# Performance work log

Measured on AMD Instinct MI355X. Metric: run time of the kernel, lower is better.

Reference implementation:

```python
import jax, jax.numpy as jnp
import numpy as np

BATCH = 64
N_NODES = 1000
SEQ = 12
FEAT = 4          # in_features_per_node // N_history
IN_CH = 48        # in_features_per_node, also GAT out_channels
HEADS = 2
OUT_FEAT = 2      # out_features_per_node
H1, H2 = 256, 128
N_TOTAL = BATCH * N_NODES
E = 1024000


def setup_inputs() -> dict:
    key = jax.random.key(0)
    ks = jax.random.split(key, 16)
    s = 0.05
    return {
        "x": jax.random.normal(ks[0], (N_TOTAL, IN_CH), jnp.float32),
        "edge_index": jax.random.randint(ks[1], (2, E), 0, N_TOTAL, jnp.int64),
        "W_gat": jax.random.normal(ks[2], (IN_CH, HEADS * IN_CH), jnp.float32) * s,
        "att_src": jax.random.normal(ks[3], (HEADS, IN_CH), jnp.float32) * s,
        "att_dst": jax.random.normal(ks[4], (HEADS, IN_CH), jnp.float32) * s,
        "gat_bias": jax.random.normal(ks[5], (IN_CH,), jnp.float32) * s,
        "W_ih1": jax.random.normal(ks[6], (4 * H1, N_NODES * FEAT), jnp.float32) * s,
        "W_hh1": jax.random.normal(ks[7], (4 * H1, H1), jnp.float32) * s,
        "b1": jnp.zeros((4 * H1,), jnp.float32),
        "W_ih2": jax.random.normal(ks[8], (4 * H2, H1), jnp.float32) * s,
        "W_hh2": jax.random.normal(ks[9], (4 * H2, H2), jnp.float32) * s,
        "b2": jnp.zeros((4 * H2,), jnp.float32),
        "W_out": jax.random.normal(ks[10], (N_NODES * OUT_FEAT, H2), jnp.float32) * s,
        "b_out": jnp.zeros((N_NODES * OUT_FEAT,), jnp.float32),
    }


def _gat_conv(x, edge_index, W_gat, att_src, att_dst, gat_bias):
    """PyG GATConv, heads=HEADS, concat=False (mean over heads), add_self_loops=True."""
    N = x.shape[0]
    h = (x @ W_gat).reshape(N, HEADS, IN_CH)              # [N,H,C]
    a_src = jnp.einsum('nhc,hc->nh', h, att_src)          # [N,H]
    a_dst = jnp.einsum('nhc,hc->nh', h, att_dst)
    loops = jnp.arange(N, dtype=edge_index.dtype)
    src = jnp.concatenate([edge_index[0], loops])         # [E+N]
    dst = jnp.concatenate([edge_index[1], loops])
    e = jax.nn.leaky_relu(a_src[src] + a_dst[dst], 0.2)   # [E+N,H]
    # segment-softmax over incoming edges of each destination node
    m = jnp.full((N, HEADS), -jnp.inf, e.dtype).at[dst].max(e)
    w = jnp.exp(e - m[dst])
    denom = jax.ops.segment_sum(w, dst, num_segments=N)
    alpha = w / (denom[dst] + 1e-16)                      # [E+N,H]
    msg = h[src] * alpha[:, :, None]                      # [E+N,H,C]
    out = jax.ops.segment_sum(msg, dst, num_segments=N)   # [N,H,C]
    return out.mean(axis=1) + gat_bias                    # [N,C]


def _lstm(x_seq, W_ih, W_hh, b):
    """Single-layer LSTM, PyTorch gate order (i,f,g,o). x_seq: [T,B,D]."""
    Hs = W_hh.shape[1]
    B = x_seq.shape[1]
    xw = jnp.einsum('tbd,gd->tbg', x_seq, W_ih) + b       # precompute input proj

    def step(carry, xt):
        h, c = carry
        g = xt + h @ W_hh.T
        i, f, gg, o = jnp.split(g, 4, axis=-1)
        i, f, o = jax.nn.sigmoid(i), jax.nn.sigmoid(f), jax.nn.sigmoid(o)
        c = f * c + i * jnp.tanh(gg)
        h = o * jnp.tanh(c)
        return (h, c), h

    h0 = jnp.zeros((B, Hs), x_seq.dtype)
    _, ys = jax.lax.scan(step, (h0, h0), xw)
    return ys                                             # [T,B,Hs]


def reference(x, edge_index, W_gat, att_src, att_dst, gat_bias,
              W_ih1, W_hh1, b1, W_ih2, W_hh2, b2, W_out, b_out):
    g = _gat_conv(x, edge_index, W_gat, att_src, att_dst, gat_bias)  # [N_total, 48]
    # (B, N_nodes, SEQ, FEAT) -> movedim(2,0) -> (SEQ, B, N_nodes*FEAT)
    g = g.reshape(BATCH, N_NODES, SEQ, FEAT)
    g = jnp.moveaxis(g, 2, 0).reshape(SEQ, BATCH, N_NODES * FEAT)
    y = _lstm(g, W_ih1, W_hh1, b1)
    y = _lstm(y, W_ih2, W_hh2, b2)
    last = y[-1]                                          # [B, H2]
    out = last @ W_out.T + b_out                          # [B, N_nodes*OUT_FEAT]
    return out.reshape(BATCH * N_NODES, OUT_FEAT)
```

## Files before the change

### kernel.cpp

```cpp
#include <hip/hip_runtime.h>
#include <hip/hip_fp16.h>
#include <math.h>

#define NTOT   64000
#define NNODE  1000
#define NBATCH 64
#define NSEQ   12
#define NE     1024000

typedef _Float16 half8 __attribute__((ext_vector_type(8)));
typedef float f32x4 __attribute__((ext_vector_type(4)));

__device__ __forceinline__ float lrelu(float x){ return x > 0.f ? x : 0.2f*x; }
__device__ __forceinline__ float sigmoidf_(float x){ return 1.f/(1.f+__expf(-x)); }

__global__ void __launch_bounds__(256) k_gat_h(const float* __restrict__ x, const float* __restrict__ Wg,
                       const float* __restrict__ att_s, const float* __restrict__ att_d,
                       __half* __restrict__ hfeat, float* __restrict__ asrc, float* __restrict__ adst){
  __shared__ __align__(16) float Ws[48*96];
  __shared__ float as_s[96], ad_s[96];
  for (int i = threadIdx.x; i < 48*96; i += 256) Ws[i] = Wg[i];
  if (threadIdx.x < 96){ as_s[threadIdx.x] = att_s[threadIdx.x]; ad_s[threadIdx.x] = att_d[threadIdx.x]; }
  __syncthreads();
  int n = blockIdx.x * 256 + threadIdx.x;
  if (n >= NTOT) return;
  float xr[48];
  const float4* xv = (const float4*)(x + (size_t)n*48);
  #pragma unroll
  for (int q = 0; q < 12; ++q){ float4 v = xv[q]; xr[q*4]=v.x; xr[q*4+1]=v.y; xr[q*4+2]=v.z; xr[q*4+3]=v.w; }
  float a0=0.f,a1=0.f,d0=0.f,d1=0.f;
  __half* hrow = hfeat + (size_t)n*96;
  float prev = 0.f;
  for (int j = 0; j < 96; ++j){
    float acc = 0.f;
    #pragma unroll
    for (int k = 0; k < 48; ++k) acc += xr[k]*Ws[k*96+j];
    if (j & 1){
      __half2 p; p.x = __float2half(prev); p.y = __float2half(acc);
      *(__half2*)(hrow + j - 1) = p;
    } else prev = acc;
    if (j < 48){ a0 += acc*as_s[j]; d0 += acc*ad_s[j]; }
    else       { a1 += acc*as_s[j]; d1 += acc*ad_s[j]; }
  }
  asrc[n*2]=a0; asrc[n*2+1]=a1; adst[n*2]=d0; adst[n*2+1]=d1;
}

__global__ void k_count(const int* __restrict__ ei, int* __restrict__ cnt){
  int e = blockIdx.x*256 + threadIdx.x;
  if (e < NE) atomicAdd(&cnt[ei[NE + e]], 1);
}

__global__ void __launch_bounds__(256) k_scan1(const int* __restrict__ cnt, int* __restrict__ wsum){
  int w = (blockIdx.x*256 + threadIdx.x) >> 6;
  int lane = threadIdx.x & 63;
  int v = cnt[w*64 + lane];
  int t = v;
  #pragma unroll
  for (int d = 1; d < 64; d <<= 1) t += __shfl_xor(t, d);
  if (lane == 0) wsum[w] = t;
}

__global__ void __launch_bounds__(1024) k_scan2(int* __restrict__ wsum){
  __shared__ int tmp[1024];
  int k = threadIdx.x;
  int v = (k < 1000) ? wsum[k] : 0;
  tmp[k] = v; __syncthreads();
  for (int d = 1; d < 1024; d <<= 1){
    int t = (k >= d) ? tmp[k-d] : 0;
    __syncthreads();
    tmp[k] += t;
    __syncthreads();
  }
  if (k < 1000) wsum[k] = tmp[k] - v;
}

__global__ void __launch_bounds__(256) k_scan3(const int* __restrict__ cnt, const int* __restrict__ wpre,
                                               int* __restrict__ offs, int* __restrict__ cursor){
  int w = (blockIdx.x*256 + threadIdx.x) >> 6;
  int lane = threadIdx.x & 63;
  int i = w*64 + lane;
  int v = cnt[i];
  int x = v;
  #pragma unroll
  for (int d = 1; d < 64; d <<= 1){
    int t = __shfl_up(x, d);
    if (lane >= d) x += t;
  }
  int excl = wpre[w] + x - v;
  offs[i] = excl; cursor[i] = excl;
  if (i == NTOT-1) offs[NTOT] = excl + v;
}

__global__ void k_scatter(const int* __restrict__ ei, int* __restrict__ cursor, int* __restrict__ csr){
  int e = blockIdx.x*256 + threadIdx.x;
  if (e < NE){
    int d = ei[NE + e], s = ei[e];
    int pos = atomicAdd(&cursor[d], 1);
    csr[pos] = s;
  }
}

__global__ void __launch_bounds__(256) k_node(const __half* __restrict__ hf, const float* __restrict__ asrc,
                      const float* __restrict__ adst, const int* __restrict__ offs,
                      const int* __restrict__ csr, const float* __restrict__ bias,
                      _Float16* __restrict__ xseqh){
  __shared__ float gsh[4][96];
  int wv = threadIdx.x >> 6, lane = threadIdx.x & 63;
  int n = blockIdx.x*4 + wv;
  int off = offs[n], deg = offs[n+1] - off;
  const float2* as2 = (const float2*)asrc;
  float2 adn = ((const float2*)adst)[n];
  float2 asn = as2[n];
  float es0 = __expf(lrelu(asn.x + adn.x));
  float es1 = __expf(lrelu(asn.y + adn.y));
  int cl = (lane < 48) ? lane : lane - 48;
  bool h0 = (lane < 24);
  float wself = h0 ? es0 : es1;
  float ssum = wself;
  float2 acc;
  {
    __half2 r2 = *(const __half2*)(hf + (size_t)n*96 + 2*cl);
    float2 r = __half22float2(r2);
    acc.x = r.x*wself; acc.y = r.y*wself;
  }
  int i = 0;
  for (; i + 4 <= deg; i += 4){
    int ss[4];
    #pragma unroll
    for (int j = 0; j < 4; ++j) ss[j] = csr[off+i+j];
    float2 aa[4];
    #pragma unroll
    for (int j = 0; j < 4; ++j) aa[j] = as2[ss[j]];
    __half2 rr[4];
    #pragma unroll
    for (int j = 0; j < 4; ++j) rr[j] = *(const __half2*)(hf + (size_t)ss[j]*96 + 2*cl);
    #pragma unroll
    for (int j = 0; j < 4; ++j){
      float w0 = __expf(lrelu(aa[j].x + adn.x));
      float w1 = __expf(lrelu(aa[j].y + adn.y));
      float ws = h0 ? w0 : w1;
      float2 r = __half22float2(rr[j]);
      acc.x += r.x*ws; acc.y += r.y*ws;
      ssum += ws;
    }
  }
  for (; i < deg; ++i){
    int s = csr[off+i];
    float2 a = as2[s];
    __half2 r2 = *(const __half2*)(hf + (size_t)s*96 + 2*cl);
    float w0 = __expf(lrelu(a.x + adn.x));
    float w1 = __expf(lrelu(a.y + adn.y));
    float ws = h0 ? w0 : w1;
    float2 r = __half22float2(r2);
    acc.x += r.x*ws; acc.y += r.y*ws;
    ssum += ws;
  }
  float inv = 1.f/(ssum + 1e-16f);
  if (lane < 48){ gsh[wv][2*cl] = acc.x*inv; gsh[wv][2*cl+1] = acc.y*inv; }
  __syncthreads();
  if (lane < 48){
    float g = 0.5f*(gsh[wv][lane] + gsh[wv][48+lane]) + bias[lane];
    int b = n / 1000, node = n - b*1000;
    int t = lane >> 2, f = lane & 3;
    xseqh[((size_t)(t*64 + b))*4000 + node*4 + f] = (_Float16)g;
  }
}

__global__ void __launch_bounds__(256) k_cvt(const float* __restrict__ W, _Float16* __restrict__ dst){
  int i = blockIdx.x*256 + threadIdx.x;
  float4 v = *(const float4*)(W + (size_t)i*4);
  union { _Float16 h[4]; uint2 u; } o;
  o.h[0] = (_Float16)v.x; o.h[1] = (_Float16)v.y;
  o.h[2] = (_Float16)v.z; o.h[3] = (_Float16)v.w;
  *(uint2*)(dst + (size_t)i*4) = o.u;
}

__global__ void __launch_bounds__(256) k_gemm1h(const _Float16* __restrict__ A,
                        const _Float16* __restrict__ B, const float* __restrict__ b1,
                        float* __restrict__ xw1){
  __shared__ _Float16 As[64*40];
  __shared__ _Float16 Bs[64*40];
  int tid = threadIdx.x;
  int w = tid >> 6, l = tid & 63;
  int m0 = blockIdx.x*64, n0 = blockIdx.y*64;
  int fr = l & 15, fk = (l >> 4)*8;
  f32x4 acc0 = {0.f,0.f,0.f,0.f}, acc1 = acc0, acc2 = acc0, acc3 = acc0;
  int ra = tid >> 2, ca = (tid & 3)*8;
  const _Float16* Ap = A + (size_t)(m0+ra)*4000 + ca;
  const _Float16* Bp = B + (size_t)(n0+ra)*4000 + ca;
  _Float16* Asw = &As[ra*40 + ca];
  _Float16* Bsw = &Bs[ra*40 + ca];
  half8 pa = *(const half8*)Ap;
  half8 pb = *(const half8*)Bp;
  for (int k0 = 0; k0 < 4000; k0 += 32){
    *(half8*)Asw = pa;
    *(half8*)Bsw = pb;
    __syncthreads();
    if (k0 + 32 < 4000){
      pa = *(const half8*)(Ap + k0 + 32);
      pb = *(const half8*)(Bp + k0 + 32);
    }
    half8 af  = *(const half8*)&As[(w*16 + fr)*40 + fk];
    half8 bf0 = *(const half8*)&Bs[( 0 + fr)*40 + fk];
    half8 bf1 = *(const half8*)&Bs[(16 + fr)*40 + fk];
    half8 bf2 = *(const half8*)&Bs[(32 + fr)*40 + fk];
    half8 bf3 = *(const half8*)&Bs[(48 + fr)*40 + fk];
    acc0 = __builtin_amdgcn_mfma_f32_16x16x32_f16(af, bf0, acc0, 0, 0, 0);
    acc1 = __builtin_amdgcn_mfma_f32_16x16x32_f16(af, bf1, acc1, 0, 0, 0);
    acc2 = __builtin_amdgcn_mfma_f32_16x16x32_f16(af, bf2, acc2, 0, 0, 0);
    acc3 = __builtin_amdgcn_mfma_f32_16x16x32_f16(af, bf3, acc3, 0, 0, 0);
    __syncthreads();
  }
  int mrow = m0 + w*16 + (l >> 4)*4;
  int ncol = n0 + (l & 15);
  float bb0 = b1[ncol], bb1 = b1[ncol+16], bb2 = b1[ncol+32], bb3 = b1[ncol+48];
  #pragma unroll
  for (int r = 0; r < 4; ++r){
    float* cp = xw1 + (size_t)(mrow + r)*1024 + ncol;
    cp[0]  = acc0[r] + bb0;
    cp[16] = acc1[r] + bb1;
    cp[32] = acc2[r] + bb2;
    cp[48] = acc3[r] + bb3;
  }
}

__global__ void __launch_bounds__(256) k_trh(const float* __restrict__ Whh1, const float* __restrict__ Wih2,
                    const float* __restrict__ Whh2, __half* __restrict__ dst){
  int i = blockIdx.x*256 + threadIdx.x;
  if (i < 262144){ int q = i>>10, r = i&1023; dst[i] = __float2half(Whh1[r*256+q]); return; }
  i -= 262144;
  if (i < 131072){ int q = i>>9, r = i&511; dst[262144+i] = __float2half(Wih2[r*256+q]); return; }
  i -= 131072;
  if (i < 65536){ int q = i>>9, r = i&511; dst[393216+i] = __float2half(Whh2[(size_t)r*128+q]); }
}

__global__ void __launch_bounds__(1024) k_lstm(
    const float* __restrict__ xw1, const __half* __restrict__ W1,
    const __half* __restrict__ W2i, const __half* __restrict__ W2h,
    const float* __restrict__ b2, float* __restrict__ h2o){
  __shared__ float h1s[256];
  __shared__ float h2s[128];
  __shared__ __align__(16) float pbuf[8192];
  int t = threadIdx.x;
  int b = blockIdx.x;
  int kk1 = t >> 7, c1c = (t & 127) * 8;
  int kk2 = t >> 6, c2c = (t & 63) * 8;
  float cc1 = 0.f, cc2 = 0.f;
  float b2r[4] = {0.f,0.f,0.f,0.f};
  if (t < 128){
    #pragma unroll
    for (int gi = 0; gi < 4; ++gi) b2r[gi] = b2[gi*128 + t];
  }
  if (t < 256) h1s[t] = 0.f;
  if (t < 128) h2s[t] = 0.f;
  __syncthreads();

  for (int step = 0; step < NSEQ; ++step){
    {
      float acc[8] = {0,0,0,0,0,0,0,0};
      const __half* wp = W1 + (size_t)(kk1*32)*1024 + c1c;
      const float* hb = &h1s[kk1*32];
      #pragma unroll 4
      for (int q = 0; q < 32; ++q){
        uint4 wv = *(const uint4*)(wp + (size_t)q*1024);
        const __half2* hp = (const __half2*)&wv;
        float hq = hb[q];
        float2 f0 = __half22float2(hp[0]);
        float2 f1 = __half22float2(hp[1]);
        float2 f2 = __half22float2(hp[2]);
        float2 f3 = __half22float2(hp[3]);
        acc[0] += f0.x*hq; acc[1] += f0.y*hq;
        acc[2] += f1.x*hq; acc[3] += f1.y*hq;
        acc[4] += f2.x*hq; acc[5] += f2.y*hq;
        acc[6] += f3.x*hq; acc[7] += f3.y*hq;
      }
      float4 w0; w0.x=acc[0]; w0.y=acc[1]; w0.z=acc[2]; w0.w=acc[3];
      float4 w1; w1.x=acc[4]; w1.y=acc[5]; w1.z=acc[6]; w1.w=acc[7];
      *(float4*)&pbuf[kk1*1024 + c1c]     = w0;
      *(float4*)&pbuf[kk1*1024 + c1c + 4] = w1;
    }
    __syncthreads();
    if (t < 256){
      const float* xr = xw1 + ((size_t)step*64 + b)*1024 + t;
      float g[4];
      #pragma unroll
      for (int gi = 0; gi < 4; ++gi){
        float s = xr[gi*256];
        #pragma unroll
        for (int kk = 0; kk < 8; ++kk) s += pbuf[kk*1024 + gi*256 + t];
        g[gi] = s;
      }
      float i_ = sigmoidf_(g[0]);
      float f_ = sigmoidf_(g[1]);
      float gg = tanhf(g[2]);
      float o_ = sigmoidf_(g[3]);
      cc1 = f_*cc1 + i_*gg;
      h1s[t] = o_*tanhf(cc1);
    }
    __syncthreads();
    {
      float acc[8] = {0,0,0,0,0,0,0,0};
      const __half* wi = W2i + (size_t)(kk2*16)*512 + c2c;
      const float* hb1 = &h1s[kk2*16];
      #pragma unroll 4
      for (int q = 0; q < 16; ++q){
        uint4 wv = *(const uint4*)(wi + (size_t)q*512);
        const __half2* hp = (const __half2*)&wv;
        float hq = hb1[q];
        float2 f0 = __half22float2(hp[0]);
        float2 f1 = __half22float2(hp[1]);
        float2 f2 = __half22float2(hp[2]);
        float2 f3 = __half22float2(hp[3]);
        acc[0] += f0.x*hq; acc[1] += f0.y*hq;
        acc[2] += f1.x*hq; acc[3] += f1.y*hq;
        acc[4] += f2.x*hq; acc[5] += f2.y*hq;
        acc[6] += f3.x*hq; acc[7] += f3.y*hq;
      }
      const __half* wh = W2h + (size_t)(kk2*8)*512 + c2c;
      const float* hb2 = &h2s[kk2*8];
      #pragma unroll 4
      for (int q = 0; q < 8; ++q){
        uint4 wv = *(const uint4*)(wh + (size_t)q*512);
        const __half2* hp = (const __half2*)&wv;
        float hq = hb2[q];
        float2 f0 = __half22float2(hp[0]);
        float2 f1 = __half22float2(hp[1]);
        float2 f2 = __half22float2(hp[2]);
        float2 f3 = __half22float2(hp[3]);
        acc[0] += f0.x*hq; acc[1] += f0.y*hq;
        acc[2] += f1.x*hq; acc[3] += f1.y*hq;
        acc[4] += f2.x*hq; acc[5] += f2.y*hq;
        acc[6] += f3.x*hq; acc[7] += f3.y*hq;
      }
      float4 w0; w0.x=acc[0]; w0.y=acc[1]; w0.z=acc[2]; w0.w=acc[3];
      float4 w1; w1.x=acc[4]; w1.y=acc[5]; w1.z=acc[6]; w1.w=acc[7];
      *(float4*)&pbuf[kk2*512 + c2c]     = w0;
      *(float4*)&pbuf[kk2*512 + c2c + 4] = w1;
    }
    __syncthreads();
    if (t < 128){
      float g[4];
      #pragma unroll
      for (int gi = 0; gi < 4; ++gi){
        float s = b2r[gi];
        #pragma unroll
        for (int kk = 0; kk < 16; ++kk) s += pbuf[kk*512 + gi*128 + t];
        g[gi] = s;
      }
      float i_ = sigmoidf_(g[0]);
      float f_ = sigmoidf_(g[1]);
      float gg = tanhf(g[2]);
      float o_ = sigmoidf_(g[3]);
      cc2 = f_*cc2 + i_*gg;
      h2s[t] = o_*tanhf(cc2);
    }
    __syncthreads();
  }
  if (t < 128) h2o[(size_t)b*128 + t] = h2s[t];
}

__global__ void __launch_bounds__(256) k_out(const float* __restrict__ h2, const float* __restrict__ Wout,
                     const float* __restrict__ bout, float* __restrict__ out){
  __shared__ __align__(16) float hs[8][128];
  int t = threadIdx.x;
  int b0 = blockIdx.y * 8;
  #pragma unroll
  for (int r = 0; r < 4; ++r){
    int idx = r*256 + t;
    hs[idx >> 7][idx & 127] = h2[(size_t)(b0 + (idx >> 7))*128 + (idx & 127)];
  }
  __syncthreads();
  if (t >= 250) return;
  int j = blockIdx.x*250 + t;
  const float4* w = (const float4*)(Wout + (size_t)j*128);
  float bj = bout[j];
  float d[8];
  #pragma unroll
  for (int bb = 0; bb < 8; ++bb) d[bb] = bj;
  for (int q = 0; q < 32; ++q){
    float4 wv = w[q];
    #pragma unroll
    for (int bb = 0; bb < 8; ++bb){
      float4 hv = ((const float4*)hs[bb])[q];
      d[bb] += wv.x*hv.x + wv.y*hv.y + wv.z*hv.z + wv.w*hv.w;
    }
  }
  #pragma unroll
  for (int bb = 0; bb < 8; ++bb)
    out[(size_t)(b0+bb)*2000 + j] = d[bb];
}

extern "C" void kernel_launch(void* const* d_in, const int* in_sizes, int n_in,
                              void* d_out, int out_size, void* d_ws, size_t ws_size,
                              hipStream_t stream){
  const float* x     = (const float*)d_in[0];
  const int*   ei    = (const int*)d_in[1];
  const float* Wg    = (const float*)d_in[2];
  const float* att_s = (const float*)d_in[3];
  const float* att_d = (const float*)d_in[4];
  const float* gb    = (const float*)d_in[5];
  const float* Wih1  = (const float*)d_in[6];
  const float* Whh1  = (const float*)d_in[7];
  const float* b1    = (const float*)d_in[8];
  const float* Wih2  = (const float*)d_in[9];
  const float* Whh2  = (const float*)d_in[10];
  const float* b2    = (const float*)d_in[11];
  const float* Wout  = (const float*)d_in[12];
  const float* bout  = (const float*)d_in[13];
  float* out = (float*)d_out;

  char* w = (char*)d_ws;
  _Float16* xseqh = (_Float16*)w;
  char*  hbase = w + 12288000;
  __half* hfeath = (__half*)hbase;
  _Float16* Bh  = (_Float16*)hbase;
  float* xw1    = (float*)(hbase + 8192000);
  __half* W1h   = (__half*)(hbase + 11337728);
  float* h2o    = (float*)(hbase + 12255232);
  char*  p2 = w + 12288000 + 24576000;
  float* asrc   = (float*)(p2);
  float* adst   = (float*)(p2 + 512000);
  int*   cnt    = (int*)(p2 + 1024000);
  int*   offs   = (int*)(p2 + 1280000);
  int*   cursor = (int*)(p2 + 1536256);
  int*   csr    = (int*)(p2 + 1792256);
  int*   wsum   = csr;

  hipMemsetAsync(cnt, 0, NTOT*sizeof(int), stream);

  k_gat_h<<<250, 256, 0, stream>>>(x, Wg, att_s, att_d, hfeath, asrc, adst);
  k_count<<<4000, 256, 0, stream>>>(ei, cnt);
  k_scan1<<<250, 256, 0, stream>>>(cnt, wsum);
  k_scan2<<<1, 1024, 0, stream>>>(wsum);
  k_scan3<<<250, 256, 0, stream>>>(cnt, wsum, offs, cursor);
  k_scatter<<<4000, 256, 0, stream>>>(ei, cursor, csr);
  k_node<<<16000, 256, 0, stream>>>(hfeath, asrc, adst, offs, csr, gb, xseqh);

  k_cvt<<<4000, 256, 0, stream>>>(Wih1, Bh);
  k_trh<<<1792, 256, 0, stream>>>(Whh1, Wih2, Whh2, W1h);
  k_gemm1h<<<dim3(12,16), 256, 0, stream>>>(xseqh, Bh, b1, xw1);

  k_lstm<<<NBATCH, 1024, 0, stream>>>(xw1, W1h, W1h + 262144, W1h + 393216, b2, h2o);
  k_out<<<dim3(8,8), 256, 0, stream>>>(h2o, Wout, bout, out);
}
```

Before: 421.7 us.

## Wavefront-pipeline the two LSTM layers and merge the weight-prep kernels

The LSTM kernel now skews the two layers: at iteration k, layer 1 runs step k while layer 2 runs step k-1 on the previous h1. Separate partial-sum buffers let both matvecs share one barrier, cutting the barriers per step from four to two. The layer-2 gate update moves to threads 256-383 so it runs in parallel with the layer-1 gate update. The xw1 loads are issued before the matvec to hide their latency. The two weight-conversion kernels are merged into one launch. The cost is 32KB more shared memory and more live registers per thread.

```diff
diff --git a/kernel.cpp b/kernel.cpp
--- a/kernel.cpp
+++ b/kernel.cpp
@@ -166,13 +166,26 @@
   }
 }
 
-__global__ void __launch_bounds__(256) k_cvt(const float* __restrict__ W, _Float16* __restrict__ dst){
-  int i = blockIdx.x*256 + threadIdx.x;
-  float4 v = *(const float4*)(W + (size_t)i*4);
-  union { _Float16 h[4]; uint2 u; } o;
-  o.h[0] = (_Float16)v.x; o.h[1] = (_Float16)v.y;
-  o.h[2] = (_Float16)v.z; o.h[3] = (_Float16)v.w;
-  *(uint2*)(dst + (size_t)i*4) = o.u;
+__global__ void __launch_bounds__(256) k_prep(const float* __restrict__ Wih1,
+                    const float* __restrict__ Whh1, const float* __restrict__ Wih2,
+                    const float* __restrict__ Whh2,
+                    _Float16* __restrict__ Bh, __half* __restrict__ dst){
+  int blk = blockIdx.x;
+  if (blk < 4000){
+    int i = blk*256 + threadIdx.x;
+    float4 v = *(const float4*)(Wih1 + (size_t)i*4);
+    union { _Float16 h[4]; uint2 u; } o;
+    o.h[0] = (_Float16)v.x; o.h[1] = (_Float16)v.y;
+    o.h[2] = (_Float16)v.z; o.h[3] = (_Float16)v.w;
+    *(uint2*)(Bh + (size_t)i*4) = o.u;
+    return;
+  }
+  int i = (blk-4000)*256 + threadIdx.x;
+  if (i < 262144){ int q = i>>10, r = i&1023; dst[i] = __float2half(Whh1[r*256+q]); return; }
+  i -= 262144;
+  if (i < 131072){ int q = i>>9, r = i&511; dst[262144+i] = __float2half(Wih2[r*256+q]); return; }
+  i -= 131072;
+  if (i < 65536){ int q = i>>9, r = i&511; dst[393216+i] = __float2half(Whh2[(size_t)r*128+q]); }
 }
 
 __global__ void __launch_bounds__(256) k_gemm1h(const _Float16* __restrict__ A,
@@ -224,14 +237,16 @@
   }
 }
 
-__global__ void __launch_bounds__(256) k_trh(const float* __restrict__ Whh1, const float* __restrict__ Wih2,
-                    const float* __restrict__ Whh2, __half* __restrict__ dst){
-  int i = blockIdx.x*256 + threadIdx.x;
-  if (i < 262144){ int q = i>>10, r = i&1023; dst[i] = __float2half(Whh1[r*256+q]); return; }
-  i -= 262144;
-  if (i < 131072){ int q = i>>9, r = i&511; dst[262144+i] = __float2half(Wih2[r*256+q]); return; }
-  i -= 131072;
-  if (i < 65536){ int q = i>>9, r = i&511; dst[393216+i] = __float2half(Whh2[(size_t)r*128+q]); }
+__device__ __forceinline__ void mac8(float* acc, uint4 wv, float hq){
+  const __half2* hp = (const __half2*)&wv;
+  float2 f0 = __half22float2(hp[0]);
+  float2 f1 = __half22float2(hp[1]);
+  float2 f2 = __half22float2(hp[2]);
+  float2 f3 = __half22float2(hp[3]);
+  acc[0] += f0.x*hq; acc[1] += f0.y*hq;
+  acc[2] += f1.x*hq; acc[3] += f1.y*hq;
+  acc[4] += f2.x*hq; acc[5] += f2.y*hq;
+  acc[6] += f3.x*hq; acc[7] += f3.y*hq;
 }
 
 __global__ void __launch_bounds__(1024) k_lstm(
@@ -240,54 +255,67 @@
     const float* __restrict__ b2, float* __restrict__ h2o){
   __shared__ float h1s[256];
   __shared__ float h2s[128];
-  __shared__ __align__(16) float pbuf[8192];
+  __shared__ __align__(16) float pA[8192];
+  __shared__ __align__(16) float pB[8192];
   int t = threadIdx.x;
   int b = blockIdx.x;
   int kk1 = t >> 7, c1c = (t & 127) * 8;
   int kk2 = t >> 6, c2c = (t & 63) * 8;
+  int u2 = t - 256;
   float cc1 = 0.f, cc2 = 0.f;
   float b2r[4] = {0.f,0.f,0.f,0.f};
-  if (t < 128){
-    #pragma unroll
-    for (int gi = 0; gi < 4; ++gi) b2r[gi] = b2[gi*128 + t];
+  if (t >= 256 && t < 384){
+    #pragma unroll
+    for (int gi = 0; gi < 4; ++gi) b2r[gi] = b2[gi*128 + u2];
   }
   if (t < 256) h1s[t] = 0.f;
   if (t < 128) h2s[t] = 0.f;
   __syncthreads();
 
-  for (int step = 0; step < NSEQ; ++step){
-    {
+  for (int k = 0; k <= NSEQ; ++k){
+    float xg[4] = {0.f,0.f,0.f,0.f};
+    if (k < NSEQ && t < 256){
+      const float* xr = xw1 + ((size_t)k*64 + b)*1024 + t;
+      #pragma unroll
+      for (int gi = 0; gi < 4; ++gi) xg[gi] = xr[gi*256];
+    }
+    if (k < NSEQ){
       float acc[8] = {0,0,0,0,0,0,0,0};
       const __half* wp = W1 + (size_t)(kk1*32)*1024 + c1c;
       const float* hb = &h1s[kk1*32];
       #pragma unroll 4
-      for (int q = 0; q < 32; ++q){
-        uint4 wv = *(const uint4*)(wp + (size_t)q*1024);
-        const __half2* hp = (const __half2*)&wv;
-        float hq = hb[q];
-        float2 f0 = __half22float2(hp[0]);
-        float2 f1 = __half22float2(hp[1]);
-        float2 f2 = __half22float2(hp[2]);
-        float2 f3 = __half22float2(hp[3]);
-        acc[0] += f0.x*hq; acc[1] += f0.y*hq;
-        acc[2] += f1.x*hq; acc[3] += f1.y*hq;
-        acc[4] += f2.x*hq; acc[5] += f2.y*hq;
-        acc[6] += f3.x*hq; acc[7] += f3.y*hq;
-      }
+      for (int q = 0; q < 32; ++q)
+        mac8(acc, *(const uint4*)(wp + (size_t)q*1024), hb[q]);
       float4 w0; w0.x=acc[0]; w0.y=acc[1]; w0.z=acc[2]; w0.w=acc[3];
       float4 w1; w1.x=acc[4]; w1.y=acc[5]; w1.z=acc[6]; w1.w=acc[7];
-      *(float4*)&pbuf[kk1*1024 + c1c]     = w0;
-      *(float4*)&pbuf[kk1*1024 + c1c + 4] = w1;
-    }
-    __syncthreads();
-    if (t < 256){
-      const float* xr = xw1 + ((size_t)step*64 + b)*1024 + t;
+      *(float4*)&pA[kk1*1024 + c1c]     = w0;
+      *(float4*)&pA[kk1*1024 + c1c + 4] = w1;
+    }
+    if (k >= 1){
+      float acch[8] = {0,0,0,0,0,0,0,0};
+      const __half* wi = W2i + (size_t)(kk2*16)*512 + c2c;
+      const float* hb1 = &h1s[kk2*16];
+      #pragma unroll 4
+      for (int q = 0; q < 16; ++q)
+        mac8(acch, *(const uint4*)(wi + (size_t)q*512), hb1[q]);
+      const __half* wh = W2h + (size_t)(kk2*8)*512 + c2c;
+      const float* hb2 = &h2s[kk2*8];
+      #pragma unroll 4
+      for (int q = 0; q < 8; ++q)
+        mac8(acch, *(const uint4*)(wh + (size_t)q*512), hb2[q]);
+      float4 w0; w0.x=acch[0]; w0.y=acch[1]; w0.z=acch[2]; w0.w=acch[3];
+      float4 w1; w1.x=acch[4]; w1.y=acch[5]; w1.z=acch[6]; w1.w=acch[7];
+      *(float4*)&pB[kk2*512 + c2c]     = w0;
+      *(float4*)&pB[kk2*512 + c2c + 4] = w1;
+    }
+    __syncthreads();
+    if (k < NSEQ && t < 256){
       float g[4];
       #pragma unroll
       for (int gi = 0; gi < 4; ++gi){
-        float s = xr[gi*256];
+        float s = xg[gi];
         #pragma unroll
-        for (int kk = 0; kk < 8; ++kk) s += pbuf[kk*1024 + gi*256 + t];
+        for (int kk = 0; kk < 8; ++kk) s += pA[kk*1024 + gi*256 + t];
         g[gi] = s;
       }
       float i_ = sigmoidf_(g[0]);
@@ -297,54 +325,13 @@
       cc1 = f_*cc1 + i_*gg;
       h1s[t] = o_*tanhf(cc1);
     }
-    __syncthreads();
-    {
-      float acc[8] = {0,0,0,0,0,0,0,0};
-      const __half* wi = W2i + (size_t)(kk2*16)*512 + c2c;
-      const float* hb1 = &h1s[kk2*16];
-      #pragma unroll 4
-      for (int q = 0; q < 16; ++q){
-        uint4 wv = *(const uint4*)(wi + (size_t)q*512);
-        const __half2* hp = (const __half2*)&wv;
-        float hq = hb1[q];
-        float2 f0 = __half22float2(hp[0]);
-        float2 f1 = __half22float2(hp[1]);
-        float2 f2 = __half22float2(hp[2]);
-        float2 f3 = __half22float2(hp[3]);
-        acc[0] += f0.x*hq; acc[1] += f0.y*hq;
-        acc[2] += f1.x*hq; acc[3] += f1.y*hq;
-        acc[4] += f2.x*hq; acc[5] += f2.y*hq;
-        acc[6] += f3.x*hq; acc[7] += f3.y*hq;
-      }
-      const __half* wh = W2h + (size_t)(kk2*8)*512 + c2c;
-      const float* hb2 = &h2s[kk2*8];
-      #pragma unroll 4
-      for (int q = 0; q < 8; ++q){
-        uint4 wv = *(const uint4*)(wh + (size_t)q*512);
-        const __half2* hp = (const __half2*)&wv;
-        float hq = hb2[q];
-        float2 f0 = __half22float2(hp[0]);
-        float2 f1 = __half22float2(hp[1]);
-        float2 f2 = __half22float2(hp[2]);
-        float2 f3 = __half22float2(hp[3]);
-        acc[0] += f0.x*hq; acc[1] += f0.y*hq;
-        acc[2] += f1.x*hq; acc[3] += f1.y*hq;
-        acc[4] += f2.x*hq; acc[5] += f2.y*hq;
-        acc[6] += f3.x*hq; acc[7] += f3.y*hq;
-      }
-      float4 w0; w0.x=acc[0]; w0.y=acc[1]; w0.z=acc[2]; w0.w=acc[3];
-      float4 w1; w1.x=acc[4]; w1.y=acc[5]; w1.z=acc[6]; w1.w=acc[7];
-      *(float4*)&pbuf[kk2*512 + c2c]     = w0;
-      *(float4*)&pbuf[kk2*512 + c2c + 4] = w1;
-    }
-    __syncthreads();
-    if (t < 128){
+    if (k >= 1 && t >= 256 && t < 384){
       float g[4];
       #pragma unroll
       for (int gi = 0; gi < 4; ++gi){
         float s = b2r[gi];
         #pragma unroll
-        for (int kk = 0; kk < 16; ++kk) s += pbuf[kk*512 + gi*128 + t];
+        for (int kk = 0; kk < 16; ++kk) s += pB[kk*512 + gi*128 + u2];
         g[gi] = s;
       }
       float i_ = sigmoidf_(g[0]);
@@ -352,11 +339,11 @@
       float gg = tanhf(g[2]);
       float o_ = sigmoidf_(g[3]);
       cc2 = f_*cc2 + i_*gg;
-      h2s[t] = o_*tanhf(cc2);
-    }
-    __syncthreads();
-  }
-  if (t < 128) h2o[(size_t)b*128 + t] = h2s[t];
+      h2s[u2] = o_*tanhf(cc2);
+    }
+    __syncthreads();
+  }
+  if (t >= 256 && t < 384) h2o[(size_t)b*128 + u2] = h2s[u2];
 }
 
 __global__ void __launch_bounds__(256) k_out(const float* __restrict__ h2, const float* __restrict__ Wout,
@@ -436,8 +423,7 @@
   k_scatter<<<4000, 256, 0, stream>>>(ei, cursor, csr);
   k_node<<<16000, 256, 0, stream>>>(hfeath, asrc, adst, offs, csr, gb, xseqh);
 
-  k_cvt<<<4000, 256, 0, stream>>>(Wih1, Bh);
-  k_trh<<<1792, 256, 0, stream>>>(Whh1, Wih2, Whh2, W1h);
+  k_prep<<<5792, 256, 0, stream>>>(Wih1, Whh1, Wih2, Whh2, Bh, W1h);
   k_gemm1h<<<dim3(12,16), 256, 0, stream>>>(xseqh, Bh, b1, xw1);
 
   k_lstm<<<NBATCH, 1024, 0, stream>>>(xw1, W1h, W1h + 262144, W1h + 393216, b2, h2o);
```

Result: faster. 409.2 us (-3.0%).
